# Optimization experiments

Hardware: AMD Instinct MI355X
Metric: run time of the kernel (lower is better)

## Reference

```python
import jax, jax.numpy as jnp
import numpy as np

GAMMA = 1.0

def setup_inputs() -> dict:
    key = jax.random.key(0)
    k1, k2 = jax.random.split(key)
    pred = jax.random.normal(k1, (8, 2048, 8), dtype=jnp.float32)
    target = jax.random.normal(k2, (8, 2048, 8), dtype=jnp.float32)
    return {"pred": pred, "target": target}

def reference(pred, target):
    # pairwise squared distances dist[b,i,j] = sum_f (pred[b,i,f]-target[b,j,f])^2
    # computed as ||p||^2 + ||t||^2 - 2 p.t to avoid materializing (B,L,L,F)
    p2 = jnp.sum(pred * pred, axis=-1)            # (B, L)
    t2 = jnp.sum(target * target, axis=-1)        # (B, L)
    pt = jnp.einsum('bif,bjf->bij', pred, target) # (B, L, L)
    distances = p2[:, :, None] + t2[:, None, :] - 2.0 * pt
    # soft-min over target positions: -gamma * logsumexp(-d/gamma)
    min_distances = -GAMMA * jax.nn.logsumexp(-distances / GAMMA, axis=-1)
    return jnp.mean(min_distances)
```

## Files before the change

kernel.cpp:

```cpp
#include <hip/hip_runtime.h>
#include <math.h>

#define BATCH 8
#define LEN   2048
#define FEAT  8
#define MROWS 32
#define THREADS 512
#define JO    (LEN / 8)
#define NCHUNK (JO / 16)
#define NBLK  (BATCH * (LEN / MROWS))
#define LOG2E 1.4426950408889634f
#define LN2   0.6931471805599453f
#define P2S   (2.0f * LOG2E)

typedef _Float16 f16x8 __attribute__((ext_vector_type(8)));
typedef float    f32x4 __attribute__((ext_vector_type(4)));

__device__ __forceinline__ float exp2_hw(float x) {
    float d; asm("v_exp_f32 %0, %1" : "=v"(d) : "v"(x)); return d;
}
__device__ __forceinline__ float log2_hw(float x) {
    float d; asm("v_log_f32 %0, %1" : "=v"(d) : "v"(x)); return d;
}

template <bool ATOMIC>
__global__ __launch_bounds__(THREADS, 4) void dtw_mfma(
    const float* __restrict__ pred, const float* __restrict__ target,
    float* __restrict__ partial_or_out)
{
    __shared__ f16x8 s_t16[LEN];
    __shared__ float s_mt2[LEN];
    __shared__ float s_red[MROWS * 8];
    __shared__ float s_qp[MROWS];

    const int tid = threadIdx.x;
    const int b   = blockIdx.x / (LEN / MROWS);
    const int rs  = blockIdx.x % (LEN / MROWS);
    const int jo  = tid >> 6;
    const int ln  = tid & 63;
    const int col = ln & 15;
    const int g   = ln >> 4;
    const int i0  = rs * MROWS;

    const float4* t4 = (const float4*)(target + (size_t)b * LEN * FEAT);
    #pragma unroll
    for (int u = 0; u < LEN / THREADS; ++u) {
        const int jj = u * THREADS + tid;
        float4 ta = t4[(size_t)jj * 2];
        float4 tb = t4[(size_t)jj * 2 + 1];
        f16x8 h;
        h[0] = (_Float16)ta.x; h[1] = (_Float16)ta.y;
        h[2] = (_Float16)ta.z; h[3] = (_Float16)ta.w;
        h[4] = (_Float16)tb.x; h[5] = (_Float16)tb.y;
        h[6] = (_Float16)tb.z; h[7] = (_Float16)tb.w;
        float t2 = 0.f;
        #pragma unroll
        for (int e = 0; e < 8; ++e) { float f = (float)h[e]; t2 += f * f; }
        s_t16[jj] = h;
        s_mt2[jj] = -LOG2E * t2;
    }

    f16x8 afrag0, afrag1;
    #pragma unroll
    for (int e = 0; e < 8; ++e) { afrag0[e] = (_Float16)0.f;
                                  afrag1[e] = (_Float16)0.f; }
    {
        const float* pb = pred + ((size_t)b * LEN + i0 + col) * FEAT;
        const float4* pA = (const float4*)pb;
        const float4* pB = (const float4*)(pb + 16 * FEAT);
        float4 a0 = pA[0], c0 = pA[1], a1 = pB[0], c1 = pB[1];
        float f0[8] = {a0.x, a0.y, a0.z, a0.w, c0.x, c0.y, c0.z, c0.w};
        float f1[8] = {a1.x, a1.y, a1.z, a1.w, c1.x, c1.y, c1.z, c1.w};
        f16x8 r0, r1;
        float e0 = 0.f, e1 = 0.f;
        #pragma unroll
        for (int e = 0; e < 8; ++e) {
            r0[e] = (_Float16)(P2S * f0[e]);
            r1[e] = (_Float16)(P2S * f1[e]);
            float x0 = (float)r0[e], x1 = (float)r1[e];
            e0 += x0 * x0; e1 += x1 * x1;
        }
        if (g == 0) { afrag0 = r0; afrag1 = r1; }
        if (jo == 0 && g == 0) {
            s_qp[col]      = e0 * (0.25f / LOG2E);
            s_qp[16 + col] = e1 * (0.25f / LOG2E);
        }
    }

    __syncthreads();

    const int jbase = jo * JO;
    f32x4 acc0 = {0.f, 0.f, 0.f, 0.f};
    f32x4 acc1 = {0.f, 0.f, 0.f, 0.f};
    const f32x4 Z = {0.f, 0.f, 0.f, 0.f};
    #pragma unroll
    for (int ch = 0; ch < NCHUNK; ++ch) {
        const int j0 = jbase + ch * 16;
        f16x8 bfrag = s_t16[j0 + col];
        float mt2c  = s_mt2[j0 + col];
        f32x4 S0 = __builtin_amdgcn_mfma_f32_16x16x32_f16(
            afrag0, bfrag, Z, 0, 0, 0);
        f32x4 S1 = __builtin_amdgcn_mfma_f32_16x16x32_f16(
            afrag1, bfrag, Z, 0, 0, 0);
        #pragma unroll
        for (int r = 0; r < 4; ++r) {
            acc0[r] += exp2_hw(S0[r] + mt2c);
            acc1[r] += exp2_hw(S1[r] + mt2c);
        }
    }

    #pragma unroll
    for (int m = 1; m < 16; m <<= 1) {
        #pragma unroll
        for (int r = 0; r < 4; ++r) {
            acc0[r] += __shfl_xor(acc0[r], m);
            acc1[r] += __shfl_xor(acc1[r], m);
        }
    }
    if (col == 0) {
        #pragma unroll
        for (int r = 0; r < 4; ++r) {
            s_red[(g * 4 + r) * 8 + jo]        = acc0[r];
            s_red[(16 + g * 4 + r) * 8 + jo]   = acc1[r];
        }
    }
    __syncthreads();

    if (tid < MROWS) {
        float s = 0.f;
        #pragma unroll
        for (int q = 0; q < 8; ++q) s += s_red[tid * 8 + q];
        float v = log2_hw(s) - s_qp[tid];
        v += __shfl_xor(v, 1);
        v += __shfl_xor(v, 2);
        v += __shfl_xor(v, 4);
        v += __shfl_xor(v, 8);
        v += __shfl_xor(v, 16);
        if (tid == 0) {
            float tot = -LN2 * v;
            if (ATOMIC) {
                atomicAdd(partial_or_out, tot * (1.0f / (BATCH * LEN)));
            } else {
                partial_or_out[blockIdx.x] = tot;
            }
        }
    }
}

__global__ __launch_bounds__(256) void dtw_reduce(
    const float* __restrict__ partial, float* __restrict__ out)
{
    __shared__ float s_w[4];
    const int tid = threadIdx.x;
    float v = partial[tid] + partial[tid + 256];
    v += __shfl_xor(v, 1);
    v += __shfl_xor(v, 2);
    v += __shfl_xor(v, 4);
    v += __shfl_xor(v, 8);
    v += __shfl_xor(v, 16);
    v += __shfl_xor(v, 32);
    if ((tid & 63) == 0) s_w[tid >> 6] = v;
    __syncthreads();
    if (tid == 0)
        out[0] = (s_w[0] + s_w[1] + s_w[2] + s_w[3]) * (1.0f / (BATCH * LEN));
}

extern "C" void kernel_launch(void* const* d_in, const int* in_sizes, int n_in,
                              void* d_out, int out_size, void* d_ws, size_t ws_size,
                              hipStream_t stream) {
    const float* pred   = (const float*)d_in[0];
    const float* target = (const float*)d_in[1];
    float* out = (float*)d_out;

    if (ws_size >= NBLK * sizeof(float)) {
        float* partial = (float*)d_ws;
        dtw_mfma<false><<<NBLK, THREADS, 0, stream>>>(pred, target, partial);
        dtw_reduce<<<1, 256, 0, stream>>>(partial, out);
    } else {
        hipMemsetAsync(d_out, 0, sizeof(float), stream);
        dtw_mfma<true><<<NBLK, THREADS, 0, stream>>>(pred, target, out);
    }
}
```

Measured before the change: 14.42 us.

## Double rows per block to 64 with 16 waves to amortize target staging

```diff
diff --git a/kernel.cpp b/kernel.cpp
--- a/kernel.cpp
+++ b/kernel.cpp
@@ -4,10 +4,10 @@
 #define BATCH 8
 #define LEN   2048
 #define FEAT  8
-#define MROWS 32
-#define THREADS 512
-#define JO    (LEN / 8)
-#define NCHUNK (JO / 16)
+#define MROWS 64
+#define THREADS 1024
+#define JS    (LEN / 16)
+#define NCHUNK (JS / 16)
 #define NBLK  (BATCH * (LEN / MROWS))
 #define LOG2E 1.4426950408889634f
 #define LN2   0.6931471805599453f
@@ -30,7 +30,7 @@
 {
     __shared__ f16x8 s_t16[LEN];
     __shared__ float s_mt2[LEN];
-    __shared__ float s_red[MROWS * 8];
+    __shared__ float s_red[MROWS * 16];
     __shared__ float s_qp[MROWS];
 
     const int tid = threadIdx.x;
@@ -60,52 +60,59 @@
         s_mt2[jj] = -LOG2E * t2;
     }
 
-    f16x8 afrag0, afrag1;
+    f16x8 af0, af1, af2, af3;
     #pragma unroll
-    for (int e = 0; e < 8; ++e) { afrag0[e] = (_Float16)0.f;
-                                  afrag1[e] = (_Float16)0.f; }
+    for (int e = 0; e < 8; ++e) {
+        af0[e] = (_Float16)0.f; af1[e] = (_Float16)0.f;
+        af2[e] = (_Float16)0.f; af3[e] = (_Float16)0.f;
+    }
     {
         const float* pb = pred + ((size_t)b * LEN + i0 + col) * FEAT;
-        const float4* pA = (const float4*)pb;
-        const float4* pB = (const float4*)(pb + 16 * FEAT);
-        float4 a0 = pA[0], c0 = pA[1], a1 = pB[0], c1 = pB[1];
-        float f0[8] = {a0.x, a0.y, a0.z, a0.w, c0.x, c0.y, c0.z, c0.w};
-        float f1[8] = {a1.x, a1.y, a1.z, a1.w, c1.x, c1.y, c1.z, c1.w};
-        f16x8 r0, r1;
-        float e0 = 0.f, e1 = 0.f;
         #pragma unroll
-        for (int e = 0; e < 8; ++e) {
-            r0[e] = (_Float16)(P2S * f0[e]);
-            r1[e] = (_Float16)(P2S * f1[e]);
-            float x0 = (float)r0[e], x1 = (float)r1[e];
-            e0 += x0 * x0; e1 += x1 * x1;
-        }
-        if (g == 0) { afrag0 = r0; afrag1 = r1; }
-        if (jo == 0 && g == 0) {
-            s_qp[col]      = e0 * (0.25f / LOG2E);
-            s_qp[16 + col] = e1 * (0.25f / LOG2E);
+        for (int f = 0; f < 4; ++f) {
+            const float4* pf4 = (const float4*)(pb + f * 16 * FEAT);
+            float4 a = pf4[0], c = pf4[1];
+            float pf[8] = {a.x, a.y, a.z, a.w, c.x, c.y, c.z, c.w};
+            f16x8 r;
+            float e2 = 0.f;
+            #pragma unroll
+            for (int e = 0; e < 8; ++e) {
+                r[e] = (_Float16)(P2S * pf[e]);
+                float x = (float)r[e];
+                e2 += x * x;
+            }
+            if (g == 0) {
+                if (f == 0) af0 = r;
+                else if (f == 1) af1 = r;
+                else if (f == 2) af2 = r;
+                else af3 = r;
+                if (jo == 0)
+                    s_qp[f * 16 + col] = e2 * (0.25f / LOG2E);
+            }
         }
     }
 
     __syncthreads();
 
-    const int jbase = jo * JO;
-    f32x4 acc0 = {0.f, 0.f, 0.f, 0.f};
-    f32x4 acc1 = {0.f, 0.f, 0.f, 0.f};
+    const int jbase = jo * JS;
+    f32x4 ac0 = {0.f,0.f,0.f,0.f}, ac1 = {0.f,0.f,0.f,0.f};
+    f32x4 ac2 = {0.f,0.f,0.f,0.f}, ac3 = {0.f,0.f,0.f,0.f};
     const f32x4 Z = {0.f, 0.f, 0.f, 0.f};
     #pragma unroll
     for (int ch = 0; ch < NCHUNK; ++ch) {
         const int j0 = jbase + ch * 16;
         f16x8 bfrag = s_t16[j0 + col];
         float mt2c  = s_mt2[j0 + col];
-        f32x4 S0 = __builtin_amdgcn_mfma_f32_16x16x32_f16(
-            afrag0, bfrag, Z, 0, 0, 0);
-        f32x4 S1 = __builtin_amdgcn_mfma_f32_16x16x32_f16(
-            afrag1, bfrag, Z, 0, 0, 0);
+        f32x4 S0 = __builtin_amdgcn_mfma_f32_16x16x32_f16(af0, bfrag, Z, 0,0,0);
+        f32x4 S1 = __builtin_amdgcn_mfma_f32_16x16x32_f16(af1, bfrag, Z, 0,0,0);
+        f32x4 S2 = __builtin_amdgcn_mfma_f32_16x16x32_f16(af2, bfrag, Z, 0,0,0);
+        f32x4 S3 = __builtin_amdgcn_mfma_f32_16x16x32_f16(af3, bfrag, Z, 0,0,0);
         #pragma unroll
         for (int r = 0; r < 4; ++r) {
-            acc0[r] += exp2_hw(S0[r] + mt2c);
-            acc1[r] += exp2_hw(S1[r] + mt2c);
+            ac0[r] += exp2_hw(S0[r] + mt2c);
+            ac1[r] += exp2_hw(S1[r] + mt2c);
+            ac2[r] += exp2_hw(S2[r] + mt2c);
+            ac3[r] += exp2_hw(S3[r] + mt2c);
         }
     }
 
@@ -113,15 +120,19 @@
     for (int m = 1; m < 16; m <<= 1) {
         #pragma unroll
         for (int r = 0; r < 4; ++r) {
-            acc0[r] += __shfl_xor(acc0[r], m);
-            acc1[r] += __shfl_xor(acc1[r], m);
+            ac0[r] += __shfl_xor(ac0[r], m);
+            ac1[r] += __shfl_xor(ac1[r], m);
+            ac2[r] += __shfl_xor(ac2[r], m);
+            ac3[r] += __shfl_xor(ac3[r], m);
         }
     }
     if (col == 0) {
         #pragma unroll
         for (int r = 0; r < 4; ++r) {
-            s_red[(g * 4 + r) * 8 + jo]        = acc0[r];
-            s_red[(16 + g * 4 + r) * 8 + jo]   = acc1[r];
+            s_red[(g * 4 + r) * 16 + jo]      = ac0[r];
+            s_red[(16 + g * 4 + r) * 16 + jo] = ac1[r];
+            s_red[(32 + g * 4 + r) * 16 + jo] = ac2[r];
+            s_red[(48 + g * 4 + r) * 16 + jo] = ac3[r];
         }
     }
     __syncthreads();
@@ -129,13 +140,14 @@
     if (tid < MROWS) {
         float s = 0.f;
         #pragma unroll
-        for (int q = 0; q < 8; ++q) s += s_red[tid * 8 + q];
+        for (int q = 0; q < 16; ++q) s += s_red[tid * 16 + q];
         float v = log2_hw(s) - s_qp[tid];
         v += __shfl_xor(v, 1);
         v += __shfl_xor(v, 2);
         v += __shfl_xor(v, 4);
         v += __shfl_xor(v, 8);
         v += __shfl_xor(v, 16);
+        v += __shfl_xor(v, 32);
         if (tid == 0) {
             float tot = -LN2 * v;
             if (ATOMIC) {
@@ -152,7 +164,7 @@
 {
     __shared__ float s_w[4];
     const int tid = threadIdx.x;
-    float v = partial[tid] + partial[tid + 256];
+    float v = partial[tid];
     v += __shfl_xor(v, 1);
     v += __shfl_xor(v, 2);
     v += __shfl_xor(v, 4);
```

Result: slower. 15.87 us (+10.0%).
